# Performance work log

Measured on AMD Instinct MI355X. Metric: run time of the kernel, lower is better.

The kernel has to match this reference:

```python
import jax, jax.numpy as jnp
import numpy as np

D_MODEL = 1024
EXPAND = 2
D_INNER = EXPAND * D_MODEL  # 2048
HEADDIM = 64
NHEADS = D_INNER // HEADDIM  # 32
D_STATE = 64
D_CONV = 4
BATCH = 2
SEQ_LEN = 1024
LN_EPS = 1e-5


def setup_inputs() -> dict:
    key = jax.random.key(0)
    ks = jax.random.split(key, 12)
    s = 0.02
    return {
        "hidden_states": jax.random.normal(ks[0], (BATCH, SEQ_LEN, D_MODEL), jnp.float32),
        "in_proj_w": jax.random.normal(ks[1], (2 * D_INNER, D_MODEL), jnp.float32) * s,
        "conv_w": jax.random.normal(ks[2], (D_INNER, 1, D_CONV), jnp.float32) * 0.1,
        "conv_b": jax.random.normal(ks[3], (D_INNER,), jnp.float32) * 0.01,
        "A_log": jnp.zeros((NHEADS,), jnp.float32),  # log(ones) as in init
        "dt_w": jax.random.normal(ks[4], (NHEADS, D_INNER), jnp.float32) * s,
        "dt_b": jax.random.normal(ks[5], (NHEADS,), jnp.float32) * 0.1,
        "B_w": jax.random.normal(ks[6], (NHEADS * D_STATE, D_INNER), jnp.float32) * s,
        "C_w": jax.random.normal(ks[7], (NHEADS * D_STATE, D_INNER), jnp.float32) * s,
        "D": jnp.ones((NHEADS,), jnp.float32),
        "ln_w": jnp.ones((D_INNER,), jnp.float32),
        "ln_b": jnp.zeros((D_INNER,), jnp.float32),
        "out_proj_w": jax.random.normal(ks[8], (D_MODEL, D_INNER), jnp.float32) * s,
    }


def _layernorm(x, w, b):
    mu = jnp.mean(x, axis=-1, keepdims=True)
    var = jnp.var(x, axis=-1, keepdims=True)
    return (x - mu) * jax.lax.rsqrt(var + LN_EPS) * w + b


def _forward(hidden_states, in_proj_w, conv_w, conv_b, A_log, dt_w, dt_b,
             B_w, C_w, D, ln_w, ln_b, out_proj_w):
    B_, L, _ = hidden_states.shape
    xz = hidden_states @ in_proj_w.T                       # [B, L, 2*d_inner]
    x, z = jnp.split(xz, 2, axis=-1)

    # depthwise causal conv1d (torch pads both sides, slices [:L] == causal left-pad)
    x_ncl = jnp.transpose(x, (0, 2, 1))                    # [B, d_inner, L]
    x_conv = jax.lax.conv_general_dilated(
        x_ncl, conv_w, window_strides=(1,), padding=[(D_CONV - 1, 0)],
        dimension_numbers=("NCH", "OIH", "NCH"), feature_group_count=D_INNER)
    x_conv = x_conv + conv_b[None, :, None]
    x = jnp.transpose(x_conv, (0, 2, 1))                   # [B, L, d_inner]
    x = jax.nn.silu(x)

    dt = jax.nn.softplus(x @ dt_w.T + dt_b)                # [B, L, H]
    Bm = (x @ B_w.T).reshape(B_, L, NHEADS, D_STATE)       # [B, L, H, N]
    Cm = (x @ C_w.T).reshape(B_, L, NHEADS, D_STATE)       # [B, L, H, N]
    xh = x.reshape(B_, L, NHEADS, HEADDIM)                 # [B, L, H, P]
    A = -jnp.exp(A_log)                                    # [H]

    h0 = jnp.zeros((B_, NHEADS, HEADDIM, D_STATE), x.dtype)

    def step(h, inp):
        x_t, dt_t, B_t, C_t = inp  # [B,H,P], [B,H], [B,H,N], [B,H,N]
        A_bar = jnp.exp(A[None, :] * dt_t)[..., None, None]           # [B,H,1,1]
        h = A_bar * h + (dt_t[..., None, None] * B_t[:, :, None, :]) * x_t[..., None]
        y_t = jnp.einsum("bhpn,bhn->bhp", h, C_t) + D[None, :, None] * x_t
        return h, y_t

    xs = (jnp.transpose(xh, (1, 0, 2, 3)), jnp.transpose(dt, (1, 0, 2)),
          jnp.transpose(Bm, (1, 0, 2, 3)), jnp.transpose(Cm, (1, 0, 2, 3)))
    h_final, y = jax.lax.scan(step, h0, xs)                # y: [L, B, H, P]
    y = jnp.transpose(y, (1, 0, 2, 3)).reshape(B_, L, D_INNER)

    y = _layernorm(y, ln_w, ln_b)
    y = y * jax.nn.silu(z)
    output = y @ out_proj_w.T
    return output, h_final


def reference(hidden_states, in_proj_w, conv_w, conv_b, A_log, dt_w, dt_b,
              B_w, C_w, D, ln_w, ln_b, out_proj_w):
    return _forward(hidden_states, in_proj_w, conv_w, conv_b, A_log, dt_w, dt_b,
                    B_w, C_w, D, ln_w, ln_b, out_proj_w)
```

## Files before the change

### kernel.cpp

```cpp
#include <hip/hip_runtime.h>
#include <math.h>

#define BATCH 2
#define SEQLEN 1024
#define DMODEL 1024
#define DINNER 2048
#define NHEADS 32
#define HEADDIM 64
#define DSTATE 64
#define NTOK (BATCH * SEQLEN)
#define OUT_ELEMS (BATCH * SEQLEN * DMODEL)
#define NCHUNK 16
#define LDP 72

typedef unsigned short bf16u;
typedef __attribute__((ext_vector_type(8))) short short8;
typedef __attribute__((ext_vector_type(4))) float f32x4;

__device__ __forceinline__ float b2f(short u) {
  return __uint_as_float(((unsigned)(unsigned short)u) << 16);
}
__device__ __forceinline__ unsigned short f2b(float f) {
  unsigned u = __float_as_uint(f);
  u += 0x7fff + ((u >> 16) & 1);
  return (unsigned short)(u >> 16);
}

__device__ __forceinline__ void gload16(const void* g, void* l) {
  __builtin_amdgcn_global_load_lds(
      (const __attribute__((address_space(1))) unsigned int*)g,
      (__attribute__((address_space(3))) unsigned int*)l, 16, 0, 0);
}

__device__ __forceinline__ void stv(float* p, float v) { *p = v; }
__device__ __forceinline__ void stv(bf16u* p, float v) { *p = f2b(v); }

__global__ __launch_bounds__(256) void cvt_all(
    const float* __restrict__ s0, bf16u* __restrict__ d0,
    const float* __restrict__ s1, bf16u* __restrict__ d1,
    const float* __restrict__ s2, bf16u* __restrict__ d2,
    const float* __restrict__ s3, bf16u* __restrict__ d3,
    const float* __restrict__ s4, bf16u* __restrict__ d4,
    const float* __restrict__ s5, bf16u* __restrict__ d5) {
  const size_t M1 = 1u << 20;
  size_t i = (size_t)(blockIdx.x * 256 + threadIdx.x) * 8;
  const float* src; bf16u* dst; size_t off;
  if (i < 2 * M1)       { src = s0; dst = d0; off = i; }
  else if (i < 6 * M1)  { src = s1; dst = d1; off = i - 2 * M1; }
  else if (i < 10 * M1) { src = s2; dst = d2; off = i - 6 * M1; }
  else if (i < 14 * M1) { src = s3; dst = d3; off = i - 10 * M1; }
  else if (i < 16 * M1) { src = s4; dst = d4; off = i - 14 * M1; }
  else if (i < 16 * M1 + 65536) { src = s5; dst = d5; off = i - 16 * M1; }
  else return;
  const float4 a = *(const float4*)(src + off);
  const float4 b = *(const float4*)(src + off + 4);
  short8 o;
  o[0] = f2b(a.x); o[1] = f2b(a.y); o[2] = f2b(a.z); o[3] = f2b(a.w);
  o[4] = f2b(b.x); o[5] = f2b(b.y); o[6] = f2b(b.z); o[7] = f2b(b.w);
  *(short8*)(dst + off) = o;
}

template <typename OutT>
__global__ __launch_bounds__(256) void gemm_mfma(
    const bf16u* __restrict__ A, const bf16u* __restrict__ B,
    OutT* __restrict__ C, int M, int N, int Ksub, int lda, int ldb,
    size_t zstrideC) {
  __shared__ bf16u sA[3][128 * 32];
  __shared__ bf16u sB[3][64 * 32];
  const int t = threadIdx.x;
  const int lane = t & 63, wave = t >> 6;
  const int nwg = gridDim.x * gridDim.y;
  const int fid = blockIdx.y * gridDim.x + blockIdx.x;
  const int tile = (fid & 7) * (nwg >> 3) + (fid >> 3);
  const int bm = (tile % gridDim.y) * 128;
  const int bn = (tile / gridDim.y) * 64;
  const int wr = wave >> 1, wc = wave & 1;
  const int kbase = blockIdx.z * Ksub;
  OutT* Cz = C + (size_t)blockIdx.z * zstrideC;

  const int ra0 = bm + (t >> 2), ra1 = bm + 64 + (t >> 2);
  int rb0 = bn + (t >> 2);
  rb0 = rb0 < N ? rb0 : N - 1;
  const int kc = (((t & 3) ^ ((t >> 4) & 3))) * 8;

  const bf16u* Ap0 = A + (size_t)ra0 * lda + kbase + kc;
  const bf16u* Ap1 = A + (size_t)ra1 * lda + kbase + kc;
  const bf16u* Bp0 = B + (size_t)rb0 * ldb + kbase + kc;
  const int ldsoff = (wave * 64) * 8;

#define STAGE(buf, k0)                                   \
  do {                                                   \
    gload16(Ap0 + (k0), sA[buf] + ldsoff);               \
    gload16(Ap1 + (k0), sA[buf] + 2048 + ldsoff);        \
    gload16(Bp0 + (k0), sB[buf] + ldsoff);               \
  } while (0)

  const f32x4 zero = {0.f, 0.f, 0.f, 0.f};
  f32x4 acc[4][2];
#pragma unroll
  for (int m = 0; m < 4; ++m)
#pragma unroll
    for (int n = 0; n < 2; ++n) acc[m][n] = zero;

  const int ln15 = lane & 15, kq = lane >> 4;
  const int kswz = ((kq ^ ((ln15 >> 2) & 3))) * 8;
  const int nt = Ksub >> 5;

  STAGE(0, 0);
  STAGE(1, 32);
  int curb = 0;
  for (int it = 0; it < nt; ++it) {
    if (it + 2 < nt) {
      const int nb = (it + 2) % 3;
      STAGE(nb, (it + 2) * 32);
      asm volatile("s_waitcnt vmcnt(3)" ::: "memory");
    } else {
      asm volatile("s_waitcnt vmcnt(0)" ::: "memory");
    }
    const bf16u* pA = sA[curb];
    const bf16u* pB = sB[curb];
    short8 af[4], bfr[2];
#pragma unroll
    for (int m = 0; m < 4; ++m)
      af[m] = *(const short8*)&pA[(wr * 64 + m * 16 + ln15) * 32 + kswz];
#pragma unroll
    for (int n = 0; n < 2; ++n)
      bfr[n] = *(const short8*)&pB[(wc * 32 + n * 16 + ln15) * 32 + kswz];
    asm volatile("s_waitcnt lgkmcnt(0)" ::: "memory");
    __builtin_amdgcn_sched_barrier(0);
    __builtin_amdgcn_s_barrier();
    __builtin_amdgcn_s_setprio(1);
#pragma unroll
    for (int m = 0; m < 4; ++m)
#pragma unroll
      for (int n = 0; n < 2; ++n)
        acc[m][n] = __builtin_amdgcn_mfma_f32_16x16x32_bf16(af[m], bfr[n], acc[m][n], 0, 0, 0);
    __builtin_amdgcn_s_setprio(0);
    curb = (curb == 2) ? 0 : curb + 1;
  }
#undef STAGE

  const int rbase = bm + wr * 64, cbase = bn + wc * 32;
#pragma unroll
  for (int m = 0; m < 4; ++m) {
#pragma unroll
    for (int n = 0; n < 2; ++n) {
      const int col = cbase + n * 16 + ln15;
      if (col < N) {
#pragma unroll
        for (int r = 0; r < 4; ++r) {
          const int row = rbase + m * 16 + kq * 4 + r;
          stv(&Cz[(size_t)row * N + col], acc[m][n][r]);
        }
      }
    }
  }
}

__global__ __launch_bounds__(256) void add_f32(const float* __restrict__ a,
                                               const float* __restrict__ b,
                                               float* __restrict__ o, int n) {
  const int i = (blockIdx.x * 256 + threadIdx.x) * 4;
  if (i >= n) return;
  const float4 x = *(const float4*)(a + i);
  const float4 y = *(const float4*)(b + i);
  *(float4*)(o + i) = make_float4(x.x + y.x, x.y + y.y, x.z + y.z, x.w + y.w);
}

__global__ __launch_bounds__(256) void conv_silu(
    const bf16u* __restrict__ xzb, const float* __restrict__ cw,
    const float* __restrict__ cb, bf16u* __restrict__ xcb) {
  const int i = blockIdx.x * 256 + threadIdx.x;
  const int c8 = (i & 255) * 8;
  const int tok = i >> 8;
  const int l = tok & (SEQLEN - 1);
  const bf16u* xp = xzb + (size_t)tok * (2 * DINNER) + c8;
  const short8 zer = {0, 0, 0, 0, 0, 0, 0, 0};
  const short8 x0 = *(const short8*)xp;
  const short8 x1 = (l >= 1) ? *(const short8*)(xp - 1 * (2 * DINNER)) : zer;
  const short8 x2 = (l >= 2) ? *(const short8*)(xp - 2 * (2 * DINNER)) : zer;
  const short8 x3 = (l >= 3) ? *(const short8*)(xp - 3 * (2 * DINNER)) : zer;
  short8 ob;
#pragma unroll
  for (int j = 0; j < 8; ++j) {
    const float4 w = *(const float4*)(cw + (c8 + j) * 4);
    float acc = cb[c8 + j] + w.w * b2f(x0[j]);
    acc += w.z * b2f(x1[j]);
    acc += w.y * b2f(x2[j]);
    acc += w.x * b2f(x3[j]);
    const float s = acc / (1.f + __expf(-acc));
    ob[j] = (short)f2b(s);
  }
  *(short8*)(xcb + (size_t)tok * DINNER + c8) = ob;
}

__global__ __launch_bounds__(256) void chunk_intra(
    const bf16u* __restrict__ xcb, const bf16u* __restrict__ BCb,
    const float* __restrict__ dtp8, const float* __restrict__ dt_b,
    const float* __restrict__ A_log,
    bf16u* __restrict__ ybb, float* __restrict__ Sbuf,
    float* __restrict__ rbuf, float* __restrict__ lambuf) {
  __shared__ bf16u sC[64 * LDP], sB[64 * LDP], sXT[64 * LDP];
  __shared__ bf16u sWBT[64 * LDP], sP[64 * LDP];
  __shared__ float sS[64], sDt[64], sW[64];

  const int blk = blockIdx.x;
  const int bh = blk >> 4, c = blk & (NCHUNK - 1);
  const int b = bh >> 5, h = bh & (NHEADS - 1);
  const int t = threadIdx.x, lane = t & 63, wave = t >> 6;
  const int t0 = b * SEQLEN + c * 64;
  const size_t rowbase = (size_t)t0 * DINNER + h * 64;
  const size_t rowBC = (size_t)t0 * 4096 + h * 64;

  if (wave == 0) {
    const size_t di = (size_t)(t0 + lane) * NHEADS + h;
    float dr = dt_b[h];
#pragma unroll
    for (int k = 0; k < 8; ++k) dr += dtp8[di + (size_t)k * 65536];
    const float dtv = (dr > 20.f) ? dr : log1pf(__expf(dr));
    const float Ah = -__expf(A_log[h]);
    float s = Ah * dtv;
#pragma unroll
    for (int off = 1; off < 64; off <<= 1) {
      const float o = __shfl_up(s, off);
      if (lane >= off) s += o;
    }
    const float stot = __shfl(s, 63);
    sS[lane] = s;
    sDt[lane] = dtv;
    sW[lane] = __expf(stot - s) * dtv;
    rbuf[(size_t)blk * 64 + lane] = __expf(s);
    if (lane == 0) lambuf[blk] = __expf(stot);
  } else if (wave == 1) {
#pragma unroll
    for (int it = 0; it < 8; ++it) {
      const int slot = it * 64 + lane;
      const int r = slot >> 3, c8 = (slot & 7) * 8;
      *(short8*)&sC[r * LDP + c8] =
          *(const short8*)&BCb[rowBC + 2048 + (size_t)r * 4096 + c8];
    }
  } else if (wave == 2) {
#pragma unroll
    for (int it = 0; it < 8; ++it) {
      const int slot = it * 64 + lane;
      const int r = slot >> 3, c8 = (slot & 7) * 8;
      *(short8*)&sB[r * LDP + c8] =
          *(const short8*)&BCb[rowBC + (size_t)r * 4096 + c8];
    }
  } else {
#pragma unroll
    for (int it = 0; it < 8; ++it) {
      const int slot = it * 64 + lane;
      const int j = slot >> 3, p0 = (slot & 7) * 8;
      const short8 v = *(const short8*)&xcb[rowbase + (size_t)j * DINNER + p0];
#pragma unroll
      for (int k = 0; k < 8; ++k) sXT[(p0 + k) * LDP + j] = v[k];
    }
  }
  __syncthreads();

  {
    const int j = t >> 2, n0 = (t & 3) * 16;
    const float wj = sW[j];
#pragma unroll
    for (int k = 0; k < 16; ++k)
      sWBT[(n0 + k) * LDP + j] = f2b(wj * b2f(sB[j * LDP + n0 + k]));
  }
  const int ln15 = lane & 15, kq = lane >> 4;
  const int i0 = wave * 16;
  const f32x4 zero = {0.f, 0.f, 0.f, 0.f};
  {
    f32x4 g[4];
#pragma unroll
    for (int jf = 0; jf < 4; ++jf) g[jf] = zero;
#pragma unroll
    for (int k0 = 0; k0 < 64; k0 += 32) {
      const short8 a = *(const short8*)&sC[(i0 + ln15) * LDP + k0 + kq * 8];
#pragma unroll
      for (int jf = 0; jf < 4; ++jf) {
        const short8 bb = *(const short8*)&sB[(jf * 16 + ln15) * LDP + k0 + kq * 8];
        g[jf] = __builtin_amdgcn_mfma_f32_16x16x32_bf16(a, bb, g[jf], 0, 0, 0);
      }
    }
#pragma unroll
    for (int jf = 0; jf < 4; ++jf) {
      const int j = jf * 16 + ln15;
      const float sj = sS[j], dtj = sDt[j];
#pragma unroll
      for (int r = 0; r < 4; ++r) {
        const int i = i0 + kq * 4 + r;
        const float v = (j <= i) ? g[jf][r] * __expf(sS[i] - sj) * dtj : 0.f;
        sP[i * LDP + j] = f2b(v);
      }
    }
  }
  __syncthreads();

  f32x4 yi[4], ss[4];
#pragma unroll
  for (int f = 0; f < 4; ++f) { yi[f] = zero; ss[f] = zero; }
#pragma unroll
  for (int k0 = 0; k0 < 64; k0 += 32) {
    const short8 ap = *(const short8*)&sP[(i0 + ln15) * LDP + k0 + kq * 8];
    const short8 ax = *(const short8*)&sXT[(i0 + ln15) * LDP + k0 + kq * 8];
#pragma unroll
    for (int f = 0; f < 4; ++f) {
      const short8 bx = *(const short8*)&sXT[(f * 16 + ln15) * LDP + k0 + kq * 8];
      const short8 bw = *(const short8*)&sWBT[(f * 16 + ln15) * LDP + k0 + kq * 8];
      yi[f] = __builtin_amdgcn_mfma_f32_16x16x32_bf16(ap, bx, yi[f], 0, 0, 0);
      ss[f] = __builtin_amdgcn_mfma_f32_16x16x32_bf16(ax, bw, ss[f], 0, 0, 0);
    }
  }
  bf16u* yb = ybb + (size_t)blk * 4096;
  float* sb = Sbuf + (size_t)blk * 4096;
#pragma unroll
  for (int f = 0; f < 4; ++f) {
#pragma unroll
    for (int r = 0; r < 4; ++r) {
      const int row = i0 + kq * 4 + r;
      const int col = f * 16 + ln15;
      yb[row * 64 + col] = f2b(yi[f][r]);
      sb[row * 64 + col] = ss[f][r];
    }
  }
}

__global__ __launch_bounds__(256) void chunk_scan(
    const float* __restrict__ Sbuf, const float* __restrict__ lambuf,
    bf16u* __restrict__ Hprevb, float* __restrict__ hf) {
  const int bh = blockIdx.x;
  const int t = threadIdx.x;
  const int e0 = t * 16;
  float H[16];
#pragma unroll
  for (int j = 0; j < 16; ++j) H[j] = 0.f;

  float4 cur[4];
  float lam;
  {
    const float4* sp = (const float4*)(Sbuf + (size_t)(bh * NCHUNK) * 4096 + e0);
#pragma unroll
    for (int q = 0; q < 4; ++q) cur[q] = sp[q];
    lam = lambuf[bh * NCHUNK];
  }
  for (int c = 0; c < NCHUNK; ++c) {
    float4 nxt[4];
    float lamn = 0.f;
    if (c < NCHUNK - 1) {
      const float4* sp = (const float4*)(Sbuf + (size_t)(bh * NCHUNK + c + 1) * 4096 + e0);
#pragma unroll
      for (int q = 0; q < 4; ++q) nxt[q] = sp[q];
      lamn = lambuf[bh * NCHUNK + c + 1];
    }
    short8 o0, o1;
#pragma unroll
    for (int j = 0; j < 8; ++j) o0[j] = (short)f2b(H[j]);
#pragma unroll
    for (int j = 0; j < 8; ++j) o1[j] = (short)f2b(H[8 + j]);
    *(short8*)&Hprevb[(size_t)(bh * NCHUNK + c) * 4096 + e0] = o0;
    *(short8*)&Hprevb[(size_t)(bh * NCHUNK + c) * 4096 + e0 + 8] = o1;
#pragma unroll
    for (int q = 0; q < 4; ++q) {
      H[q * 4 + 0] = lam * H[q * 4 + 0] + cur[q].x;
      H[q * 4 + 1] = lam * H[q * 4 + 1] + cur[q].y;
      H[q * 4 + 2] = lam * H[q * 4 + 2] + cur[q].z;
      H[q * 4 + 3] = lam * H[q * 4 + 3] + cur[q].w;
    }
#pragma unroll
    for (int q = 0; q < 4; ++q) cur[q] = nxt[q];
    lam = lamn;
  }
  float* hp = hf + (size_t)bh * 4096 + e0;
#pragma unroll
  for (int q = 0; q < 4; ++q)
    *(float4*)(hp + q * 4) =
        make_float4(H[q * 4], H[q * 4 + 1], H[q * 4 + 2], H[q * 4 + 3]);
}

__global__ __launch_bounds__(256) void chunk_inter(
    const bf16u* __restrict__ BCb, const bf16u* __restrict__ Hprevb,
    const bf16u* __restrict__ xcb, const bf16u* __restrict__ ybb,
    const float* __restrict__ rbuf, const float* __restrict__ Dvec,
    bf16u* __restrict__ yout) {
  __shared__ bf16u sC[64 * LDP], sH[64 * LDP];
  __shared__ float sR[64];
  const int blk = blockIdx.x;
  const int bh = blk >> 4, c = blk & (NCHUNK - 1);
  const int b = bh >> 5, h = bh & (NHEADS - 1);
  const int t = threadIdx.x, lane = t & 63, wave = t >> 6;
  const int t0 = b * SEQLEN + c * 64;
  const size_t rowbase = (size_t)t0 * DINNER + h * 64;
  const size_t rowBC = (size_t)t0 * 4096 + h * 64;

#pragma unroll
  for (int it = 0; it < 2; ++it) {
    const int slot = it * 256 + t;
    const int r = slot >> 3, c8 = (slot & 7) * 8;
    *(short8*)&sC[r * LDP + c8] =
        *(const short8*)&BCb[rowBC + 2048 + (size_t)r * 4096 + c8];
    *(short8*)&sH[r * LDP + c8] =
        *(const short8*)&Hprevb[(size_t)blk * 4096 + slot * 8];
  }
  if (t < 64) sR[t] = rbuf[(size_t)blk * 64 + t];
  __syncthreads();

  const int ln15 = lane & 15, kq = lane >> 4;
  const int i0 = wave * 16;
  const f32x4 zero = {0.f, 0.f, 0.f, 0.f};
  f32x4 acc[4];
#pragma unroll
  for (int f = 0; f < 4; ++f) acc[f] = zero;
#pragma unroll
  for (int k0 = 0; k0 < 64; k0 += 32) {
    const short8 a = *(const short8*)&sC[(i0 + ln15) * LDP + k0 + kq * 8];
#pragma unroll
    for (int f = 0; f < 4; ++f) {
      const short8 bh8 = *(const short8*)&sH[(f * 16 + ln15) * LDP + k0 + kq * 8];
      acc[f] = __builtin_amdgcn_mfma_f32_16x16x32_bf16(a, bh8, acc[f], 0, 0, 0);
    }
  }
  const float Dh = Dvec[h];
  const bf16u* yb = ybb + (size_t)blk * 4096;
#pragma unroll
  for (int f = 0; f < 4; ++f) {
    const int p = f * 16 + ln15;
#pragma unroll
    for (int r = 0; r < 4; ++r) {
      const int i = i0 + kq * 4 + r;
      const float xv = b2f((short)xcb[rowbase + (size_t)i * DINNER + p]);
      const float y = b2f((short)yb[i * 64 + p]) + sR[i] * acc[f][r] + Dh * xv;
      yout[rowbase + (size_t)i * DINNER + p] = f2b(y);
    }
  }
}

__global__ __launch_bounds__(256) void ln_gate(
    const bf16u* __restrict__ y, const bf16u* __restrict__ xzb,
    const float* __restrict__ lnw, const float* __restrict__ lnb,
    bf16u* __restrict__ out) {
  const int tok = blockIdx.x;
  const int t = threadIdx.x;
  const short8 yv8 = *(const short8*)(y + (size_t)tok * DINNER + t * 8);
  const short8 zv8 = *(const short8*)(xzb + (size_t)tok * (2 * DINNER) + DINNER + t * 8);
  float v[8];
  float s = 0.f, s2 = 0.f;
#pragma unroll
  for (int j = 0; j < 8; ++j) {
    v[j] = b2f(yv8[j]);
    s += v[j];
    s2 += v[j] * v[j];
  }
#pragma unroll
  for (int off = 32; off > 0; off >>= 1) {
    s += __shfl_down(s, off);
    s2 += __shfl_down(s2, off);
  }
  __shared__ float ws[4], ws2[4];
  const int wid = t >> 6;
  if ((t & 63) == 0) { ws[wid] = s; ws2[wid] = s2; }
  __syncthreads();
  const float mean = (ws[0] + ws[1] + ws[2] + ws[3]) * (1.f / DINNER);
  const float m2 = (ws2[0] + ws2[1] + ws2[2] + ws2[3]) * (1.f / DINNER);
  const float rstd = rsqrtf(m2 - mean * mean + 1e-5f);
  const float4 w0 = *(const float4*)(lnw + t * 8);
  const float4 w1 = *(const float4*)(lnw + t * 8 + 4);
  const float4 b0 = *(const float4*)(lnb + t * 8);
  const float4 b1 = *(const float4*)(lnb + t * 8 + 4);
  const float wv[8] = {w0.x, w0.y, w0.z, w0.w, w1.x, w1.y, w1.z, w1.w};
  const float bv[8] = {b0.x, b0.y, b0.z, b0.w, b1.x, b1.y, b1.z, b1.w};
  short8 o;
#pragma unroll
  for (int j = 0; j < 8; ++j) {
    const float zn = b2f(zv8[j]);
    const float gate = zn / (1.f + __expf(-zn));
    o[j] = (short)f2b(((v[j] - mean) * rstd * wv[j] + bv[j]) * gate);
  }
  *(short8*)(out + (size_t)tok * DINNER + t * 8) = o;
}

extern "C" void kernel_launch(void* const* d_in, const int* in_sizes, int n_in,
                              void* d_out, int out_size, void* d_ws, size_t ws_size,
                              hipStream_t stream) {
  const float* hidden = (const float*)d_in[0];
  const float* in_proj_w = (const float*)d_in[1];
  const float* conv_w = (const float*)d_in[2];
  const float* conv_b = (const float*)d_in[3];
  const float* A_log = (const float*)d_in[4];
  const float* dt_w = (const float*)d_in[5];
  const float* dt_b = (const float*)d_in[6];
  const float* B_w = (const float*)d_in[7];
  const float* C_w = (const float*)d_in[8];
  const float* Dv = (const float*)d_in[9];
  const float* ln_w = (const float*)d_in[10];
  const float* ln_b = (const float*)d_in[11];
  const float* out_proj_w = (const float*)d_in[12];

  float* out = (float*)d_out;
  float* f = (float*)d_ws;
  const size_t M1 = 1u << 20;

  bf16u* xzb    = (bf16u*)(f + 0);
  bf16u* xcb    = (bf16u*)(f + 4 * M1);
  bf16u* BCb    = (bf16u*)(f + 6 * M1);
  bf16u* wBCb   = (bf16u*)(f + 10 * M1);
  bf16u* ybb    = (bf16u*)(f + 10 * M1);
  float* outp   = f + 6 * M1;
  bf16u* wInb   = (bf16u*)(f + 14 * M1);
  bf16u* hiddenb= (bf16u*)(f + 16 * M1);
  bf16u* wdtb   = (bf16u*)(f + 17 * M1);
  float* Sbuf   = f + 14 * M1;
  bf16u* ygb    = (bf16u*)(f + 14 * M1);
  bf16u* yscb   = (bf16u*)(f + 16 * M1);
  bf16u* Hprevb = (bf16u*)(f + 18 * M1);
  bf16u* wOb    = (bf16u*)(f + 20 * M1);
  float* dtbuf  = f + 21 * M1;
  float* rbuf   = f + 21 * M1 + 524288;
  float* lambuf = f + 21 * M1 + 589824;

  float* hf = out + OUT_ELEMS;

  cvt_all<<<8224, 256, 0, stream>>>(hidden, hiddenb, in_proj_w, wInb,
                                    B_w, wBCb, C_w, wBCb + 4 * M1,
                                    out_proj_w, wOb, dt_w, wdtb);

  gemm_mfma<bf16u><<<dim3(64, 16, 1), 256, 0, stream>>>(
      hiddenb, wInb, xzb, NTOK, 2 * DINNER, DMODEL, DMODEL, DMODEL, 0);
  conv_silu<<<2048, 256, 0, stream>>>(xzb, conv_w, conv_b, xcb);
  gemm_mfma<float><<<dim3(1, 16, 8), 256, 0, stream>>>(
      xcb, wdtb, dtbuf, NTOK, NHEADS, DINNER / 8, DINNER, DINNER,
      (size_t)NTOK * NHEADS);
  gemm_mfma<bf16u><<<dim3(64, 16, 1), 256, 0, stream>>>(
      xcb, wBCb, BCb, NTOK, 2 * DINNER, DINNER, DINNER, DINNER, 0);
  chunk_intra<<<BATCH * NHEADS * NCHUNK, 256, 0, stream>>>(
      xcb, BCb, dtbuf, dt_b, A_log, ybb, Sbuf, rbuf, lambuf);
  chunk_scan<<<BATCH * NHEADS, 256, 0, stream>>>(Sbuf, lambuf, Hprevb, hf);
  chunk_inter<<<BATCH * NHEADS * NCHUNK, 256, 0, stream>>>(
      BCb, Hprevb, xcb, ybb, rbuf, Dv, yscb);
  ln_gate<<<NTOK, 256, 0, stream>>>(yscb, xzb, ln_w, ln_b, ygb);
  gemm_mfma<float><<<dim3(16, 16, 2), 256, 0, stream>>>(
      ygb, wOb, outp, NTOK, DMODEL, DINNER / 2, DINNER, DINNER,
      (size_t)2 * M1);
  add_f32<<<2048, 256, 0, stream>>>(outp, outp + 2 * M1, out, OUT_ELEMS);
}
```

Measured before the change: 185.3 us.

## Fuse dt projection into B/C GEMM and use atomic split-K for out_proj

Appends the dt_w rows after the B and C weights so a single GEMM produces B, C and dt columns (padded N to 4128), removing the separate split-K dt GEMM launch. chunk_intra now reads dt from the bf16 BC buffer, which lowers dt precision to bf16 before softplus. The out_proj split-K partial sums are accumulated with float atomicAdd into a pre-zeroed output instead of going through a separate add kernel, trading the add pass for a zero pass plus atomic traffic. Workspace buffers are rearranged to fit the wider BC matrix.

```diff
diff --git a/kernel.cpp b/kernel.cpp
--- a/kernel.cpp
+++ b/kernel.cpp
@@ -12,6 +12,8 @@
 #define OUT_ELEMS (BATCH * SEQLEN * DMODEL)
 #define NCHUNK 16
 #define LDP 72
+#define BCN 4128
+#define BCLD 4128
 
 typedef unsigned short bf16u;
 typedef __attribute__((ext_vector_type(8))) short short8;
@@ -60,7 +62,13 @@
   *(short8*)(dst + off) = o;
 }
 
-template <typename OutT>
+__global__ __launch_bounds__(256) void zero_f32(float* __restrict__ o, int n) {
+  const int i = (blockIdx.x * 256 + threadIdx.x) * 4;
+  if (i >= n) return;
+  *(float4*)(o + i) = make_float4(0.f, 0.f, 0.f, 0.f);
+}
+
+template <bool ATOMIC, typename OutT>
 __global__ __launch_bounds__(256) void gemm_mfma(
     const bf16u* __restrict__ A, const bf16u* __restrict__ B,
     OutT* __restrict__ C, int M, int N, int Ksub, int lda, int ldb,
@@ -150,21 +158,14 @@
 #pragma unroll
         for (int r = 0; r < 4; ++r) {
           const int row = rbase + m * 16 + kq * 4 + r;
-          stv(&Cz[(size_t)row * N + col], acc[m][n][r]);
+          if constexpr (ATOMIC)
+            atomicAdd(&Cz[(size_t)row * N + col], acc[m][n][r]);
+          else
+            stv(&Cz[(size_t)row * N + col], acc[m][n][r]);
         }
       }
     }
   }
-}
-
-__global__ __launch_bounds__(256) void add_f32(const float* __restrict__ a,
-                                               const float* __restrict__ b,
-                                               float* __restrict__ o, int n) {
-  const int i = (blockIdx.x * 256 + threadIdx.x) * 4;
-  if (i >= n) return;
-  const float4 x = *(const float4*)(a + i);
-  const float4 y = *(const float4*)(b + i);
-  *(float4*)(o + i) = make_float4(x.x + y.x, x.y + y.y, x.z + y.z, x.w + y.w);
 }
 
 __global__ __launch_bounds__(256) void conv_silu(
@@ -196,8 +197,7 @@
 
 __global__ __launch_bounds__(256) void chunk_intra(
     const bf16u* __restrict__ xcb, const bf16u* __restrict__ BCb,
-    const float* __restrict__ dtp8, const float* __restrict__ dt_b,
-    const float* __restrict__ A_log,
+    const float* __restrict__ dt_b, const float* __restrict__ A_log,
     bf16u* __restrict__ ybb, float* __restrict__ Sbuf,
     float* __restrict__ rbuf, float* __restrict__ lambuf) {
   __shared__ bf16u sC[64 * LDP], sB[64 * LDP], sXT[64 * LDP];
@@ -210,13 +210,11 @@
   const int t = threadIdx.x, lane = t & 63, wave = t >> 6;
   const int t0 = b * SEQLEN + c * 64;
   const size_t rowbase = (size_t)t0 * DINNER + h * 64;
-  const size_t rowBC = (size_t)t0 * 4096 + h * 64;
+  const size_t rowBC = (size_t)t0 * BCLD + h * 64;
 
   if (wave == 0) {
-    const size_t di = (size_t)(t0 + lane) * NHEADS + h;
-    float dr = dt_b[h];
-#pragma unroll
-    for (int k = 0; k < 8; ++k) dr += dtp8[di + (size_t)k * 65536];
+    const float dr =
+        b2f((short)BCb[(size_t)(t0 + lane) * BCLD + 4096 + h]) + dt_b[h];
     const float dtv = (dr > 20.f) ? dr : log1pf(__expf(dr));
     const float Ah = -__expf(A_log[h]);
     float s = Ah * dtv;
@@ -237,7 +235,7 @@
       const int slot = it * 64 + lane;
       const int r = slot >> 3, c8 = (slot & 7) * 8;
       *(short8*)&sC[r * LDP + c8] =
-          *(const short8*)&BCb[rowBC + 2048 + (size_t)r * 4096 + c8];
+          *(const short8*)&BCb[rowBC + 2048 + (size_t)r * BCLD + c8];
     }
   } else if (wave == 2) {
 #pragma unroll
@@ -245,7 +243,7 @@
       const int slot = it * 64 + lane;
       const int r = slot >> 3, c8 = (slot & 7) * 8;
       *(short8*)&sB[r * LDP + c8] =
-          *(const short8*)&BCb[rowBC + (size_t)r * 4096 + c8];
+          *(const short8*)&BCb[rowBC + (size_t)r * BCLD + c8];
     }
   } else {
 #pragma unroll
@@ -390,14 +388,14 @@
   const int t = threadIdx.x, lane = t & 63, wave = t >> 6;
   const int t0 = b * SEQLEN + c * 64;
   const size_t rowbase = (size_t)t0 * DINNER + h * 64;
-  const size_t rowBC = (size_t)t0 * 4096 + h * 64;
+  const size_t rowBC = (size_t)t0 * BCLD + h * 64;
 
 #pragma unroll
   for (int it = 0; it < 2; ++it) {
     const int slot = it * 256 + t;
     const int r = slot >> 3, c8 = (slot & 7) * 8;
     *(short8*)&sC[r * LDP + c8] =
-        *(const short8*)&BCb[rowBC + 2048 + (size_t)r * 4096 + c8];
+        *(const short8*)&BCb[rowBC + 2048 + (size_t)r * BCLD + c8];
     *(short8*)&sH[r * LDP + c8] =
         *(const short8*)&Hprevb[(size_t)blk * 4096 + slot * 8];
   }
@@ -502,43 +500,36 @@
   bf16u* xzb    = (bf16u*)(f + 0);
   bf16u* xcb    = (bf16u*)(f + 4 * M1);
   bf16u* BCb    = (bf16u*)(f + 6 * M1);
-  bf16u* wBCb   = (bf16u*)(f + 10 * M1);
-  bf16u* ybb    = (bf16u*)(f + 10 * M1);
-  float* outp   = f + 6 * M1;
-  bf16u* wInb   = (bf16u*)(f + 14 * M1);
-  bf16u* hiddenb= (bf16u*)(f + 16 * M1);
-  bf16u* wdtb   = (bf16u*)(f + 17 * M1);
-  float* Sbuf   = f + 14 * M1;
-  bf16u* ygb    = (bf16u*)(f + 14 * M1);
-  bf16u* yscb   = (bf16u*)(f + 16 * M1);
-  bf16u* Hprevb = (bf16u*)(f + 18 * M1);
-  bf16u* wOb    = (bf16u*)(f + 20 * M1);
-  float* dtbuf  = f + 21 * M1;
-  float* rbuf   = f + 21 * M1 + 524288;
-  float* lambuf = f + 21 * M1 + 589824;
+  bf16u* wBCb   = (bf16u*)(f + 10 * M1 + 524288);
+  bf16u* ybb    = (bf16u*)(f + 10 * M1 + 524288);
+  bf16u* ygb    = (bf16u*)(f + 12 * M1 + 524288);
+  bf16u* wInb   = (bf16u*)(f + 15 * M1);
+  bf16u* hiddenb= (bf16u*)(f + 17 * M1);
+  float* Sbuf   = f + 15 * M1;
+  bf16u* yscb   = (bf16u*)(f + 15 * M1);
+  bf16u* Hprevb = (bf16u*)(f + 19 * M1);
+  bf16u* wOb    = (bf16u*)(f + 21 * M1);
+  float* rbuf   = f + 22 * M1;
+  float* lambuf = f + 22 * M1 + 65536;
 
   float* hf = out + OUT_ELEMS;
 
   cvt_all<<<8224, 256, 0, stream>>>(hidden, hiddenb, in_proj_w, wInb,
                                     B_w, wBCb, C_w, wBCb + 4 * M1,
-                                    out_proj_w, wOb, dt_w, wdtb);
-
-  gemm_mfma<bf16u><<<dim3(64, 16, 1), 256, 0, stream>>>(
+                                    out_proj_w, wOb, dt_w, wBCb + 8 * M1);
+  zero_f32<<<2048, 256, 0, stream>>>(out, OUT_ELEMS);
+
+  gemm_mfma<false, bf16u><<<dim3(64, 16, 1), 256, 0, stream>>>(
       hiddenb, wInb, xzb, NTOK, 2 * DINNER, DMODEL, DMODEL, DMODEL, 0);
   conv_silu<<<2048, 256, 0, stream>>>(xzb, conv_w, conv_b, xcb);
-  gemm_mfma<float><<<dim3(1, 16, 8), 256, 0, stream>>>(
-      xcb, wdtb, dtbuf, NTOK, NHEADS, DINNER / 8, DINNER, DINNER,
-      (size_t)NTOK * NHEADS);
-  gemm_mfma<bf16u><<<dim3(64, 16, 1), 256, 0, stream>>>(
-      xcb, wBCb, BCb, NTOK, 2 * DINNER, DINNER, DINNER, DINNER, 0);
+  gemm_mfma<false, bf16u><<<dim3(65, 16, 1), 256, 0, stream>>>(
+      xcb, wBCb, BCb, NTOK, BCN, DINNER, DINNER, DINNER, 0);
   chunk_intra<<<BATCH * NHEADS * NCHUNK, 256, 0, stream>>>(
-      xcb, BCb, dtbuf, dt_b, A_log, ybb, Sbuf, rbuf, lambuf);
+      xcb, BCb, dt_b, A_log, ybb, Sbuf, rbuf, lambuf);
   chunk_scan<<<BATCH * NHEADS, 256, 0, stream>>>(Sbuf, lambuf, Hprevb, hf);
   chunk_inter<<<BATCH * NHEADS * NCHUNK, 256, 0, stream>>>(
       BCb, Hprevb, xcb, ybb, rbuf, Dv, yscb);
   ln_gate<<<NTOK, 256, 0, stream>>>(yscb, xzb, ln_w, ln_b, ygb);
-  gemm_mfma<float><<<dim3(16, 16, 2), 256, 0, stream>>>(
-      ygb, wOb, outp, NTOK, DMODEL, DINNER / 2, DINNER, DINNER,
-      (size_t)2 * M1);
-  add_f32<<<2048, 256, 0, stream>>>(outp, outp + 2 * M1, out, OUT_ELEMS);
-}
+  gemm_mfma<true, float><<<dim3(16, 16, 2), 256, 0, stream>>>(
+      ygb, wOb, out, NTOK, DMODEL, DINNER / 2, DINNER, DINNER, 0);
+}
```

New measurement: 212.8 us. 1.15x slower.
